# Optimization experiments

Measured on AMD Instinct MI355X. Metric: run time of the kernel, lower is better.

## Reference

```python
import jax, jax.numpy as jnp
import numpy as np

N_NODES = 50000


def setup_inputs() -> dict:
    key = jax.random.key(0)
    k1, k2, k3, k4, k5 = jax.random.split(key, 5)
    h = jax.random.normal(k1, (50000, 256), dtype=jnp.float32)
    norm = jax.random.uniform(k2, (50000, 1), dtype=jnp.float32)
    weight = jax.random.normal(k3, (256, 96), dtype=jnp.float32) * (1.0 / np.sqrt(96.0))
    src = jax.random.randint(k4, (800000,), 0, N_NODES, dtype=jnp.int64)
    dst = jax.random.randint(k5, (800000,), 0, N_NODES, dtype=jnp.int64)
    return {"h": h, "norm": norm, "weight": weight, "src": src, "dst": dst}


def reference(h, norm, weight, src, dst):
    # dense projection: [N, in] @ [in, out] -> [N, out]
    hw = jnp.matmul(h, weight)
    # pre-aggregation degree norm
    hw = hw * norm
    # copy_src + sum: gather messages from src, scatter-add into dst
    msgs = hw[src]  # [E, out]
    agg = jax.ops.segment_sum(msgs, dst, num_segments=N_NODES)
    # post-aggregation degree norm + activation
    out = jax.nn.relu(agg * norm)
    return out
```

## Files before the change

kernel.cpp:

```cpp
#include <hip/hip_runtime.h>

#define M_NODES 50000
#define KDIM    256
#define NDIM    96
#define NEDGE   800000
#define BM      64
#define GEMM_BLKS 782
#define NPB     64
#define NBUCK   782
#define CAPB    1536
#define EPB     2048
#define NBLK_SC 391
#define CONV_BLKS 6250
#define WT_BLKS 96

typedef short bf16x8 __attribute__((ext_vector_type(8)));
typedef float f32x4  __attribute__((ext_vector_type(4)));

__device__ inline unsigned short f2bf(float x) {
    unsigned u = __float_as_uint(x);
    u = (u + 0x7fffu + ((u >> 16) & 1u)) >> 16;
    return (unsigned short)u;
}
__device__ inline unsigned pack2bf(float x, float y) {
    return (unsigned)f2bf(x) | ((unsigned)f2bf(y) << 16);
}

__device__ inline void gload_lds16(const void* g, void* l) {
    __builtin_amdgcn_global_load_lds(
        (const __attribute__((address_space(1))) void*)g,
        (__attribute__((address_space(3))) void*)l, 16, 0, 0);
}

__global__ __launch_bounds__(256) void prep_kernel(
    const float* __restrict__ h, const float* __restrict__ w,
    unsigned short* __restrict__ hb, unsigned short* __restrict__ wt,
    int* __restrict__ gcursor)
{
    const int b = blockIdx.x, t = threadIdx.x;
    if (b < CONV_BLKS) {
        const int idx8 = b * 256 + t;
        const int row  = idx8 >> 5;
        const int u    = idx8 & 31;
        const float* hp = h + (size_t)row * KDIM + u * 8;
        float4 p = *reinterpret_cast<const float4*>(hp);
        float4 q = *reinterpret_cast<const float4*>(hp + 4);
        uint4 o;
        o.x = pack2bf(p.x, p.y); o.y = pack2bf(p.z, p.w);
        o.z = pack2bf(q.x, q.y); o.w = pack2bf(q.z, q.w);
        char* dst = reinterpret_cast<char*>(hb) + (size_t)row * 512
                  + ((u * 16) ^ ((row & 7) << 4));
        *reinterpret_cast<uint4*>(dst) = o;
    } else if (b < CONV_BLKS + WT_BLKS) {
        const int n = b - CONV_BLKS;
        wt[n * 256 + t] = f2bf(w[(size_t)t * NDIM + n]);
    } else {
        for (int i = t; i < NBUCK; i += 256) gcursor[i] = i * CAPB;
    }
}

__global__ __launch_bounds__(256) void fused_gemm_scatter_kernel(
    const unsigned short* __restrict__ hb, const float* __restrict__ norm,
    const unsigned short* __restrict__ wt, unsigned short* __restrict__ hwb,
    const int* __restrict__ src, const int* __restrict__ dst,
    int* __restrict__ gcursor, unsigned* __restrict__ binned)
{
    __shared__ __align__(16) char smem[81920];

    const int tid = threadIdx.x;

    if (blockIdx.x < GEMM_BLKS) {
        char* w_lds = smem;
        char* a_lds = smem + 49152;
        const int lane = tid & 63;
        const int wv   = tid >> 6;
        const int row0 = blockIdx.x * BM;

        const char* asrc = reinterpret_cast<const char*>(hb) + (size_t)row0 * 512;
#pragma unroll
        for (int it = 0; it < 8; ++it) {
            const int boff = wv * 8192 + it * 1024;
            gload_lds16(asrc + boff + lane * 16, a_lds + boff);
        }

#pragma unroll
        for (int it = 0; it < 12; ++it) {
            int idx = tid + it * 256;
            int n   = idx >> 5;
            int kb  = (idx & 31) * 16;
            uint4 v = *reinterpret_cast<const uint4*>(
                reinterpret_cast<const char*>(wt) + n * 512 + kb);
            *reinterpret_cast<uint4*>(w_lds + n * 512 + (kb ^ ((n & 7) << 4))) = v;
        }
        __syncthreads();

        f32x4 acc[6];
#pragma unroll
        for (int f = 0; f < 6; ++f) acc[f] = (f32x4){0.f, 0.f, 0.f, 0.f};

        const int ar = wv * 16 + (lane & 15);
        const int kg = lane >> 4;

#pragma unroll
        for (int s = 0; s < 8; ++s) {
            const int kb = s * 64 + kg * 16;
            bf16x8 a = *reinterpret_cast<const bf16x8*>(
                a_lds + ar * 512 + (kb ^ ((ar & 7) << 4)));
#pragma unroll
            for (int f = 0; f < 6; ++f) {
                int n = f * 16 + (lane & 15);
                bf16x8 b = *reinterpret_cast<const bf16x8*>(
                    w_lds + n * 512 + (kb ^ ((n & 7) << 4)));
                acc[f] = __builtin_amdgcn_mfma_f32_16x16x32_bf16(a, b, acc[f], 0, 0, 0);
            }
        }

        const int crow = wv * 16 + (lane >> 4) * 4;
        const int ccol = lane & 15;
#pragma unroll
        for (int r = 0; r < 4; ++r) {
            int row = row0 + crow + r;
            if (row < M_NODES) {
                float nv = norm[row];
#pragma unroll
                for (int f = 0; f < 6; ++f)
                    hwb[(size_t)row * NDIM + f * 16 + ccol] = f2bf(acc[f][r] * nv);
            }
        }
    } else {
        int* s_cnt  = reinterpret_cast<int*>(smem);
        int* s_base = s_cnt + NBUCK;
        const int blk = blockIdx.x - GEMM_BLKS;
        const int e0 = blk * EPB;
        const int e1 = (e0 + EPB < NEDGE) ? e0 + EPB : NEDGE;

        for (int i = tid; i < NBUCK; i += 256) s_cnt[i] = 0;
        __syncthreads();
        for (int e = e0 + tid; e < e1; e += 256)
            atomicAdd(&s_cnt[dst[e] >> 6], 1);
        __syncthreads();
        for (int i = tid; i < NBUCK; i += 256) {
            int c = s_cnt[i];
            s_base[i] = c ? atomicAdd(&gcursor[i], c) : 0;
        }
        __syncthreads();
        for (int i = tid; i < NBUCK; i += 256) s_cnt[i] = 0;
        __syncthreads();
        for (int e = e0 + tid; e < e1; e += 256) {
            int d = dst[e];
            int b = d >> 6;
            int pos = s_base[b] + atomicAdd(&s_cnt[b], 1);
            if (pos < (b + 1) * CAPB)
                binned[pos] = ((unsigned)(d & 63) << 16) | (unsigned)src[e];
        }
    }
}

#define ACCV(A, v)                                     \
    A[0] += __uint_as_float((v).x << 16);              \
    A[1] += __uint_as_float((v).x & 0xffff0000u);      \
    A[2] += __uint_as_float((v).y << 16);              \
    A[3] += __uint_as_float((v).y & 0xffff0000u);      \
    A[4] += __uint_as_float((v).z << 16);              \
    A[5] += __uint_as_float((v).z & 0xffff0000u);      \
    A[6] += __uint_as_float((v).w << 16);              \
    A[7] += __uint_as_float((v).w & 0xffff0000u);

__global__ __launch_bounds__(256) void csr_agg_kernel(
    const unsigned* __restrict__ binned, const int* __restrict__ gcursor,
    const unsigned short* __restrict__ hwb, const float* __restrict__ norm,
    float* __restrict__ out)
{
    __shared__ unsigned eL[CAPB];
    __shared__ unsigned short oL[CAPB];
    __shared__ int cnt[NPB];
    __shared__ int pfxE[NPB];

    const int b  = blockIdx.x;
    const int t  = threadIdx.x;
    const int e0 = b * CAPB;
    int cntE = gcursor[b] - e0;
    if (cntE > CAPB) cntE = CAPB;

    for (int i = t; i < cntE; i += 256) eL[i] = binned[e0 + i];
    if (t < NPB) cnt[t] = 0;
    __syncthreads();
    for (int i = t; i < cntE; i += 256)
        atomicAdd(&cnt[(eL[i] >> 16) & 63], 1);
    __syncthreads();
    if (t < NPB) {
        int v = cnt[t];
        int x = v;
#pragma unroll
        for (int st = 1; st < 64; st <<= 1) {
            int o = __shfl_up(x, st, 64);
            if (t >= st) x += o;
        }
        int ex = x - v;
        pfxE[t] = ex;
        cnt[t]  = ex;
    }
    __syncthreads();
    for (int i = t; i < cntE; i += 256) {
        unsigned v = eL[i];
        int d = (v >> 16) & 63;
        int p = atomicAdd(&cnt[d], 1);
        oL[p] = (unsigned short)(v & 0xffffu);
    }
    __syncthreads();

#pragma unroll
    for (int pass = 0; pass < 3; ++pass) {
        const int u     = pass * 256 + t;
        const int node  = u / 12;
        const int c8    = u - node * 12;
        const int gnode = b * NPB + node;
        if (gnode < M_NODES) {
            const int s0 = pfxE[node];
            const int s1 = cnt[node];
            float acc[8]  = {0.f, 0.f, 0.f, 0.f, 0.f, 0.f, 0.f, 0.f};
            float acc2[8] = {0.f, 0.f, 0.f, 0.f, 0.f, 0.f, 0.f, 0.f};
            int e = s0;
            for (; e + 4 <= s1; e += 4) {
                int a0 = oL[e], a1 = oL[e + 1], a2 = oL[e + 2], a3 = oL[e + 3];
                uint4 v0 = *reinterpret_cast<const uint4*>(hwb + (size_t)a0 * NDIM + c8 * 8);
                uint4 v1 = *reinterpret_cast<const uint4*>(hwb + (size_t)a1 * NDIM + c8 * 8);
                uint4 v2 = *reinterpret_cast<const uint4*>(hwb + (size_t)a2 * NDIM + c8 * 8);
                uint4 v3 = *reinterpret_cast<const uint4*>(hwb + (size_t)a3 * NDIM + c8 * 8);
                ACCV(acc, v0); ACCV(acc2, v1); ACCV(acc, v2); ACCV(acc2, v3);
            }
            for (; e < s1; ++e) {
                int a0 = oL[e];
                uint4 v0 = *reinterpret_cast<const uint4*>(hwb + (size_t)a0 * NDIM + c8 * 8);
                ACCV(acc, v0);
            }
            const float nv = norm[gnode];
            float4 o0, o1;
            o0.x = fmaxf((acc[0] + acc2[0]) * nv, 0.f);
            o0.y = fmaxf((acc[1] + acc2[1]) * nv, 0.f);
            o0.z = fmaxf((acc[2] + acc2[2]) * nv, 0.f);
            o0.w = fmaxf((acc[3] + acc2[3]) * nv, 0.f);
            o1.x = fmaxf((acc[4] + acc2[4]) * nv, 0.f);
            o1.y = fmaxf((acc[5] + acc2[5]) * nv, 0.f);
            o1.z = fmaxf((acc[6] + acc2[6]) * nv, 0.f);
            o1.w = fmaxf((acc[7] + acc2[7]) * nv, 0.f);
            float4* po = reinterpret_cast<float4*>(out + (size_t)gnode * NDIM + c8 * 8);
            po[0] = o0; po[1] = o1;
        }
    }
}

extern "C" void kernel_launch(void* const* d_in, const int* in_sizes, int n_in,
                              void* d_out, int out_size, void* d_ws, size_t ws_size,
                              hipStream_t stream)
{
    const float* h    = (const float*)d_in[0];
    const float* norm = (const float*)d_in[1];
    const float* w    = (const float*)d_in[2];
    const int*   src  = (const int*)d_in[3];
    const int*   dst  = (const int*)d_in[4];
    float* out = (float*)d_out;

    unsigned short* hwb = (unsigned short*)d_ws;
    unsigned short* wt  = hwb + (size_t)M_NODES * NDIM;
    int* gcursor = (int*)(wt + KDIM * NDIM);
    unsigned short* hb = (unsigned short*)(gcursor + 800);
    unsigned* binned = (unsigned*)(hb + (size_t)M_NODES * KDIM);

    prep_kernel<<<CONV_BLKS + WT_BLKS + 1, 256, 0, stream>>>(h, w, hb, wt, gcursor);
    fused_gemm_scatter_kernel<<<GEMM_BLKS + NBLK_SC, 256, 0, stream>>>(
        hb, norm, wt, hwb, src, dst, gcursor, binned);
    csr_agg_kernel<<<NBUCK, 256, 0, stream>>>(binned, gcursor, hwb, norm, out);
}
```

Before: 70.55 us.

## Fuse h fp32-to-bf16 conversion into GEMM blocks and interleave scatter blocks

Removes the separate pass that converts h to a swizzled bf16 copy in workspace. GEMM blocks now load fp32 h directly, convert it in registers and write it to LDS, which avoids writing and rereading a 25 MB intermediate. Block indices are interleaved so every third block does edge binning, mixing memory-bound scatter work with GEMM work on the device. The trade-off is that the async global-to-LDS load is replaced by synchronous loads plus conversion inside the GEMM blocks.

```diff
diff --git a/kernel.cpp b/kernel.cpp
--- a/kernel.cpp
+++ b/kernel.cpp
@@ -11,8 +11,7 @@
 #define CAPB    1536
 #define EPB     2048
 #define NBLK_SC 391
-#define CONV_BLKS 6250
-#define WT_BLKS 96
+#define TOT_BLKS (GEMM_BLKS + NBLK_SC)
 
 typedef short bf16x8 __attribute__((ext_vector_type(8)));
 typedef float f32x4  __attribute__((ext_vector_type(4)));
@@ -26,41 +25,20 @@
     return (unsigned)f2bf(x) | ((unsigned)f2bf(y) << 16);
 }
 
-__device__ inline void gload_lds16(const void* g, void* l) {
-    __builtin_amdgcn_global_load_lds(
-        (const __attribute__((address_space(1))) void*)g,
-        (__attribute__((address_space(3))) void*)l, 16, 0, 0);
-}
-
-__global__ __launch_bounds__(256) void prep_kernel(
-    const float* __restrict__ h, const float* __restrict__ w,
-    unsigned short* __restrict__ hb, unsigned short* __restrict__ wt,
+__global__ __launch_bounds__(256) void prep_w_kernel(
+    const float* __restrict__ w, unsigned short* __restrict__ wt,
     int* __restrict__ gcursor)
 {
     const int b = blockIdx.x, t = threadIdx.x;
-    if (b < CONV_BLKS) {
-        const int idx8 = b * 256 + t;
-        const int row  = idx8 >> 5;
-        const int u    = idx8 & 31;
-        const float* hp = h + (size_t)row * KDIM + u * 8;
-        float4 p = *reinterpret_cast<const float4*>(hp);
-        float4 q = *reinterpret_cast<const float4*>(hp + 4);
-        uint4 o;
-        o.x = pack2bf(p.x, p.y); o.y = pack2bf(p.z, p.w);
-        o.z = pack2bf(q.x, q.y); o.w = pack2bf(q.z, q.w);
-        char* dst = reinterpret_cast<char*>(hb) + (size_t)row * 512
-                  + ((u * 16) ^ ((row & 7) << 4));
-        *reinterpret_cast<uint4*>(dst) = o;
-    } else if (b < CONV_BLKS + WT_BLKS) {
-        const int n = b - CONV_BLKS;
-        wt[n * 256 + t] = f2bf(w[(size_t)t * NDIM + n]);
+    if (b < 96) {
+        wt[b * 256 + t] = f2bf(w[(size_t)t * NDIM + b]);
     } else {
         for (int i = t; i < NBUCK; i += 256) gcursor[i] = i * CAPB;
     }
 }
 
 __global__ __launch_bounds__(256) void fused_gemm_scatter_kernel(
-    const unsigned short* __restrict__ hb, const float* __restrict__ norm,
+    const float* __restrict__ h, const float* __restrict__ norm,
     const unsigned short* __restrict__ wt, unsigned short* __restrict__ hwb,
     const int* __restrict__ src, const int* __restrict__ dst,
     int* __restrict__ gcursor, unsigned* __restrict__ binned)
@@ -68,21 +46,27 @@
     __shared__ __align__(16) char smem[81920];
 
     const int tid = threadIdx.x;
-
-    if (blockIdx.x < GEMM_BLKS) {
+    const unsigned bx = blockIdx.x;
+
+    if (bx % 3 != 2) {
+        const int gid = (int)bx - (int)((bx + 1) / 3);
         char* w_lds = smem;
         char* a_lds = smem + 49152;
         const int lane = tid & 63;
         const int wv   = tid >> 6;
-        const int row0 = blockIdx.x * BM;
-
-        const char* asrc = reinterpret_cast<const char*>(hb) + (size_t)row0 * 512;
-#pragma unroll
-        for (int it = 0; it < 8; ++it) {
-            const int boff = wv * 8192 + it * 1024;
-            gload_lds16(asrc + boff + lane * 16, a_lds + boff);
-        }
-
+        const int row0 = gid * BM;
+
+#pragma unroll
+        for (int it = 0; it < 16; ++it) {
+            int idx = tid + it * 256;
+            int r   = idx >> 6;
+            int c4  = idx & 63;
+            int row = row0 + r;
+            if (row >= M_NODES) row = M_NODES - 1;
+            float4 v = *reinterpret_cast<const float4*>(h + (size_t)row * KDIM + c4 * 4);
+            uint2 p = make_uint2(pack2bf(v.x, v.y), pack2bf(v.z, v.w));
+            *reinterpret_cast<uint2*>(a_lds + r * 512 + ((c4 * 8) ^ ((r & 7) << 4))) = p;
+        }
 #pragma unroll
         for (int it = 0; it < 12; ++it) {
             int idx = tid + it * 256;
@@ -130,7 +114,7 @@
     } else {
         int* s_cnt  = reinterpret_cast<int*>(smem);
         int* s_base = s_cnt + NBUCK;
-        const int blk = blockIdx.x - GEMM_BLKS;
+        const int blk = (int)(bx / 3);
         const int e0 = blk * EPB;
         const int e1 = (e0 + EPB < NEDGE) ? e0 + EPB : NEDGE;
 
@@ -264,11 +248,10 @@
     unsigned short* hwb = (unsigned short*)d_ws;
     unsigned short* wt  = hwb + (size_t)M_NODES * NDIM;
     int* gcursor = (int*)(wt + KDIM * NDIM);
-    unsigned short* hb = (unsigned short*)(gcursor + 800);
-    unsigned* binned = (unsigned*)(hb + (size_t)M_NODES * KDIM);
-
-    prep_kernel<<<CONV_BLKS + WT_BLKS + 1, 256, 0, stream>>>(h, w, hb, wt, gcursor);
-    fused_gemm_scatter_kernel<<<GEMM_BLKS + NBLK_SC, 256, 0, stream>>>(
-        hb, norm, wt, hwb, src, dst, gcursor, binned);
+    unsigned* binned = (unsigned*)(gcursor + 800);
+
+    prep_w_kernel<<<97, 256, 0, stream>>>(w, wt, gcursor);
+    fused_gemm_scatter_kernel<<<TOT_BLKS, 256, 0, stream>>>(
+        h, norm, wt, hwb, src, dst, gcursor, binned);
     csr_agg_kernel<<<NBUCK, 256, 0, stream>>>(binned, gcursor, hwb, norm, out);
 }
```

Result: faster. 63.92 us (-9.4%).
